# Optimization experiments

Hardware: AMD Instinct MI355X
Metric: run time of the kernel (lower is better)

Reference implementation:

```python
import jax, jax.numpy as jnp
import numpy as np

RATIO = 2
GROUPS = 4


def conv1x1(x, w, b):
    # x: (B,C,H,W), w: (O,C), b: (O,)
    return jnp.einsum('bchw,oc->bohw', x, w) + b[None, :, None, None]


def pixel_unshuffle(x, r):
    # out[b, c*r*r + i*r + j, h, w] = x[b, c, h*r+i, w*r+j]  (torch semantics)
    B, C, H, W = x.shape
    x = x.reshape(B, C, H // r, r, W // r, r)
    x = x.transpose(0, 1, 3, 5, 2, 4)
    return x.reshape(B, C * r * r, H // r, W // r)


def grid_sample_bilinear_border(img, grid):
    # img: (N,C,H,W); grid: (N,Ho,Wo,2), grid[...,0]=x coord, grid[...,1]=y coord in [-1,1]
    # align_corners=False, padding_mode='border' (torch: clip coord to border, then bilinear)
    N, C, H, W = img.shape
    ix = ((grid[..., 0] + 1.0) * W - 1.0) * 0.5
    iy = ((grid[..., 1] + 1.0) * H - 1.0) * 0.5
    ix = jnp.clip(ix, 0.0, W - 1.0)
    iy = jnp.clip(iy, 0.0, H - 1.0)
    x0 = jnp.floor(ix)
    y0 = jnp.floor(iy)
    wx = (ix - x0)[:, None]  # (N,1,Ho,Wo) broadcast over C
    wy = (iy - y0)[:, None]
    x0i = x0.astype(jnp.int32)
    y0i = y0.astype(jnp.int32)
    x1i = jnp.minimum(x0i + 1, W - 1)
    y1i = jnp.minimum(y0i + 1, H - 1)
    gather = jax.vmap(lambda im, yy, xx: im[:, yy, xx])  # (C,Ho,Wo) per batch
    v00 = gather(img, y0i, x0i)
    v01 = gather(img, y0i, x1i)
    v10 = gather(img, y1i, x0i)
    v11 = gather(img, y1i, x1i)
    return (v00 * (1 - wx) * (1 - wy) + v01 * wx * (1 - wy)
            + v10 * (1 - wx) * wy + v11 * wx * wy)


def setup_inputs() -> dict:
    key = jax.random.key(0)
    k1, k2, k3 = jax.random.split(key, 3)
    B, C, H, W = 16, 64, 256, 256
    c_out = 2 * (GROUPS // RATIO ** 2)  # = 2
    x = jax.random.normal(k1, (B, C, H, W), jnp.float32)
    w_off = jax.random.normal(k2, (c_out, C), jnp.float32) * 0.001
    b_off = jnp.zeros((c_out,), jnp.float32)
    w_sc = jax.random.normal(k3, (c_out, C), jnp.float32) * 0.001
    b_sc = jnp.zeros((c_out,), jnp.float32)
    return {"x": x, "w_off": w_off, "b_off": b_off, "w_sc": w_sc, "b_sc": b_sc}


def reference(x, w_off, b_off, w_sc, b_sc):
    B, Cin, H, W = x.shape  # H,W divisible by RATIO -> replicate pad is a no-op
    # forward_lp with dyScope=True
    off = conv1x1(x, w_off, b_off)
    off = jax.nn.sigmoid(conv1x1(x, w_sc, b_sc)) * 0.5 * off
    off = pixel_unshuffle(off, RATIO)            # (B, 2*GROUPS, h, w)
    h, w = off.shape[2], off.shape[3]
    # x: 'b (c grp) h w -> (b grp) c h w'
    cg = Cin // GROUPS
    xg = x.reshape(B, cg, GROUPS, H, W).transpose(0, 2, 1, 3, 4).reshape(B * GROUPS, cg, H, W)
    # offset: 'b (grp two) h w -> (b grp) h w two'
    offg = off.reshape(B, GROUPS, 2, h, w).transpose(0, 1, 3, 4, 2).reshape(B * GROUPS, h, w, 2)
    # pos: stack(meshgrid(h_coord, w_coord)) -> channel 0 = h_coord, channel 1 = w_coord
    hc = jnp.arange(h, dtype=x.dtype) + 0.5
    wc = jnp.arange(w, dtype=x.dtype) + 0.5
    pos = jnp.stack(jnp.meshgrid(hc, wc, indexing='ij'), axis=-1)[None]  # (1,h,w,2)
    norm = jnp.array([w, h], dtype=x.dtype)  # normalizer = [w, h]
    grid = 2.0 * (pos + offg) / norm - 1.0
    out = grid_sample_bilinear_border(xg, grid)  # (B*GROUPS, cg, h, w)
    out = out.reshape(B, GROUPS, cg, h, w).transpose(0, 2, 1, 3, 4).reshape(B, Cin, h, w)
    return out, offg
```

## Files before the change

kernel.cpp:

```cpp
#include <hip/hip_runtime.h>
#include <math.h>

#define BATCH 16
#define CIN   64
#define HIN   256
#define WIN   256
#define HOUT  128
#define WOUT  128
#define NPIX  (HIN * WIN)
#define NPIXO (HOUT * WOUT)
#define OUT0_SIZE ((size_t)BATCH * CIN * HOUT * WOUT)

__global__ __launch_bounds__(256) void k_fused(
    const float* __restrict__ x,
    const float* __restrict__ w_off, const float* __restrict__ b_off,
    const float* __restrict__ w_sc,  const float* __restrict__ b_sc,
    float* __restrict__ out, float* __restrict__ offg)
{
    __shared__ float  sw[256];
    __shared__ float2 soff[4][16][17];
    __shared__ float  sval[4][16][272];

    int t = threadIdx.x;
    sw[t] = (t < 128) ? w_off[t] : w_sc[t - 128];

    int blk  = blockIdx.x;
    int b    = blk >> 6;
    int tile = blk & 63;
    int hh0  = (tile >> 3) * 16;
    int ww0  = (tile & 7) * 16;

    int row = t >> 4, col = t & 15;
    int hh = hh0 + row, ww = ww0 + col;

    const float* xb = x + (size_t)b * CIN * NPIX + (2 * hh) * WIN + 2 * ww;

    float aA0[2][2] = {{0,0},{0,0}}, aA1[2][2] = {{0,0},{0,0}};
    float aS0[2][2] = {{0,0},{0,0}}, aS1[2][2] = {{0,0},{0,0}};

    __syncthreads();

    #pragma unroll 8
    for (int c = 0; c < CIN; ++c) {
        const float* xc = xb + (size_t)c * NPIX;
        float2 r0 = *reinterpret_cast<const float2*>(xc);
        float2 r1 = *reinterpret_cast<const float2*>(xc + WIN);
        float wo0 = sw[c], wo1 = sw[64 + c], ws0 = sw[128 + c], ws1 = sw[192 + c];
        aA0[0][0] += r0.x * wo0;  aA0[0][1] += r0.y * wo0;
        aA0[1][0] += r1.x * wo0;  aA0[1][1] += r1.y * wo0;
        aA1[0][0] += r0.x * wo1;  aA1[0][1] += r0.y * wo1;
        aA1[1][0] += r1.x * wo1;  aA1[1][1] += r1.y * wo1;
        aS0[0][0] += r0.x * ws0;  aS0[0][1] += r0.y * ws0;
        aS0[1][0] += r1.x * ws0;  aS0[1][1] += r1.y * ws0;
        aS1[0][0] += r0.x * ws1;  aS1[0][1] += r0.y * ws1;
        aS1[1][0] += r1.x * ws1;  aS1[1][1] += r1.y * ws1;
    }

    float bo0 = b_off[0], bo1 = b_off[1];
    float bs0 = b_sc[0],  bs1 = b_sc[1];

    float og[4][2];
    #pragma unroll
    for (int i = 0; i < 2; ++i) {
        #pragma unroll
        for (int j = 0; j < 2; ++j) {
            float g0 = 1.0f / (1.0f + __expf(-(aS0[i][j] + bs0)));
            float g1 = 1.0f / (1.0f + __expf(-(aS1[i][j] + bs1)));
            og[i][j]     = g0 * 0.5f * (aA0[i][j] + bo0);
            og[2 + i][j] = g1 * 0.5f * (aA1[i][j] + bo1);
        }
    }

    #pragma unroll
    for (int g = 0; g < 4; ++g) {
        float2 vv = make_float2(og[g][0], og[g][1]);
        soff[g][row][col] = vv;
        size_t oi = ((size_t)((b * 4 + g) * HOUT + hh)) * WOUT + ww;
        *reinterpret_cast<float2*>(offg + 2 * oi) = vv;
    }
    __syncthreads();

    int hl = t & 15, wl = t >> 4;
    int shh = hh0 + hl, sww = ww0 + wl;
    const float* xg = x + (size_t)b * CIN * NPIX;

    #pragma unroll
    for (int g = 0; g < 4; ++g) {
        float2 off = soff[g][hl][wl];
        float ix = 2.0f * ((float)shh + 0.5f + off.x) - 0.5f;
        float iy = 2.0f * ((float)sww + 0.5f + off.y) - 0.5f;
        ix = fminf(fmaxf(ix, 0.0f), (float)(WIN - 1));
        iy = fminf(fmaxf(iy, 0.0f), (float)(HIN - 1));

        float x0f = floorf(ix), y0f = floorf(iy);
        float wx = ix - x0f, wy = iy - y0f;
        int x0 = (int)x0f, y0 = (int)y0f;
        int x1 = min(x0 + 1, WIN - 1);
        int y1 = min(y0 + 1, HIN - 1);

        float w00 = (1.0f - wx) * (1.0f - wy);
        float w01 = wx * (1.0f - wy);
        float w10 = (1.0f - wx) * wy;
        float w11 = wx * wy;

        int i00 = y0 * WIN + x0, i01 = y0 * WIN + x1;
        int i10 = y1 * WIN + x0, i11 = y1 * WIN + x1;

        const float* xgc = xg + (size_t)g * NPIX;
        #pragma unroll 4
        for (int c = 0; c < 16; ++c) {
            const float* xc = xgc + (size_t)c * 4 * NPIX;
            float v = xc[i00] * w00 + xc[i01] * w01
                    + xc[i10] * w10 + xc[i11] * w11;
            sval[g][c][hl * 17 + wl] = v;
        }
    }
    __syncthreads();

    int sh = t >> 4, sc = t & 15;
    float* ob = out + (((size_t)b * CIN) * HOUT + (hh0 + sh)) * WOUT + (ww0 + sc);
    #pragma unroll
    for (int g = 0; g < 4; ++g) {
        #pragma unroll 4
        for (int c = 0; c < 16; ++c)
            ob[(size_t)(c * 4 + g) * NPIXO] = sval[g][c][sh * 17 + sc];
    }
}

extern "C" void kernel_launch(void* const* d_in, const int* in_sizes, int n_in,
                              void* d_out, int out_size, void* d_ws, size_t ws_size,
                              hipStream_t stream) {
    const float* x     = (const float*)d_in[0];
    const float* w_off = (const float*)d_in[1];
    const float* b_off = (const float*)d_in[2];
    const float* w_sc  = (const float*)d_in[3];
    const float* b_sc  = (const float*)d_in[4];

    float* out  = (float*)d_out;
    float* offg = out + OUT0_SIZE;

    k_fused<<<1024, 256, 0, stream>>>(x, w_off, b_off, w_sc, b_sc, out, offg);
}
```

Measured before the change: 102.3 us.

## Stage transposed tile pairs in bf16 LDS and sample from shared memory

Each block now handles a pair of transposed 16x16 input tiles (p,q) and (q,p), because the reference's swapped h/w coordinate convention makes output (h,w) sample near input (2w,2h). Both tiles are staged in LDS as bf16, so the 1x1 convs and the bilinear gathers mostly read shared memory, with a global-memory fallback when a wave's samples fall outside the staged tile. Output is transposed through wave shuffles and written with nontemporal stores. The bf16 rounding of x changes the numerics of both the offsets and the sampled outputs, which risks tolerance failures. Large LDS use and the uneven triangular tile-pair grid also change occupancy and load balance.

```diff
diff --git a/kernel.cpp b/kernel.cpp
--- a/kernel.cpp
+++ b/kernel.cpp
@@ -9,121 +9,157 @@
 #define WOUT  128
 #define NPIX  (HIN * WIN)
 #define NPIXO (HOUT * WOUT)
-#define OUT0_SIZE ((size_t)BATCH * CIN * HOUT * WOUT)
+#define OUT0_SIZE ((size_t)BATCH * CIN * NPIXO)
 
-__global__ __launch_bounds__(256) void k_fused(
+#define NTILE 16
+#define NPAIR 136
+#define SQ_CH 256
+#define SQ_SZ (64 * SQ_CH)
+
+typedef __attribute__((ext_vector_type(4))) float f32x4;
+
+__device__ __forceinline__ unsigned short f2bf(float f) {
+    unsigned u = __float_as_uint(f);
+    return (unsigned short)((u + 0x7FFFu + ((u >> 16) & 1u)) >> 16);
+}
+
+__global__ __launch_bounds__(256, 2) void k_fused(
     const float* __restrict__ x,
     const float* __restrict__ w_off, const float* __restrict__ b_off,
     const float* __restrict__ w_sc,  const float* __restrict__ b_sc,
     float* __restrict__ out, float* __restrict__ offg)
 {
-    __shared__ float  sw[256];
-    __shared__ float2 soff[4][16][17];
-    __shared__ float  sval[4][16][272];
+    __shared__ unsigned short sq[2 * SQ_SZ];
+    __shared__ float soff[2][4][8][8][2];
+    __shared__ float sw[256];
 
-    int t = threadIdx.x;
+    const int t = threadIdx.x;
     sw[t] = (t < 128) ? w_off[t] : w_sc[t - 128];
 
-    int blk  = blockIdx.x;
-    int b    = blk >> 6;
-    int tile = blk & 63;
-    int hh0  = (tile >> 3) * 16;
-    int ww0  = (tile & 7) * 16;
+    int blk = blockIdx.x;
+    int b = blk / NPAIR;
+    int u = blk - b * NPAIR;
+    int p = 0;
+    while (u >= NTILE - p) { u -= NTILE - p; ++p; }
+    const int q = p + u;
+    const bool diag = (p == q);
+    const int nsq = diag ? 1 : 2;
 
-    int row = t >> 4, col = t & 15;
-    int hh = hh0 + row, ww = ww0 + col;
+    const float* xb = x + (size_t)b * CIN * NPIX;
+    const int rb[2] = {16 * p, 16 * q};
+    const int cb[2] = {16 * q, 16 * p};
 
-    const float* xb = x + (size_t)b * CIN * NPIX + (2 * hh) * WIN + 2 * ww;
-
-    float aA0[2][2] = {{0,0},{0,0}}, aA1[2][2] = {{0,0},{0,0}};
-    float aS0[2][2] = {{0,0},{0,0}}, aS1[2][2] = {{0,0},{0,0}};
-
-    __syncthreads();
-
-    #pragma unroll 8
-    for (int c = 0; c < CIN; ++c) {
-        const float* xc = xb + (size_t)c * NPIX;
-        float2 r0 = *reinterpret_cast<const float2*>(xc);
-        float2 r1 = *reinterpret_cast<const float2*>(xc + WIN);
-        float wo0 = sw[c], wo1 = sw[64 + c], ws0 = sw[128 + c], ws1 = sw[192 + c];
-        aA0[0][0] += r0.x * wo0;  aA0[0][1] += r0.y * wo0;
-        aA0[1][0] += r1.x * wo0;  aA0[1][1] += r1.y * wo0;
-        aA1[0][0] += r0.x * wo1;  aA1[0][1] += r0.y * wo1;
-        aA1[1][0] += r1.x * wo1;  aA1[1][1] += r1.y * wo1;
-        aS0[0][0] += r0.x * ws0;  aS0[0][1] += r0.y * ws0;
-        aS0[1][0] += r1.x * ws0;  aS0[1][1] += r1.y * ws0;
-        aS1[0][0] += r0.x * ws1;  aS1[0][1] += r0.y * ws1;
-        aS1[1][0] += r1.x * ws1;  aS1[1][1] += r1.y * ws1;
-    }
-
-    float bo0 = b_off[0], bo1 = b_off[1];
-    float bs0 = b_sc[0],  bs1 = b_sc[1];
-
-    float og[4][2];
-    #pragma unroll
-    for (int i = 0; i < 2; ++i) {
-        #pragma unroll
-        for (int j = 0; j < 2; ++j) {
-            float g0 = 1.0f / (1.0f + __expf(-(aS0[i][j] + bs0)));
-            float g1 = 1.0f / (1.0f + __expf(-(aS1[i][j] + bs1)));
-            og[i][j]     = g0 * 0.5f * (aA0[i][j] + bo0);
-            og[2 + i][j] = g1 * 0.5f * (aA1[i][j] + bo1);
-        }
-    }
-
-    #pragma unroll
-    for (int g = 0; g < 4; ++g) {
-        float2 vv = make_float2(og[g][0], og[g][1]);
-        soff[g][row][col] = vv;
-        size_t oi = ((size_t)((b * 4 + g) * HOUT + hh)) * WOUT + ww;
-        *reinterpret_cast<float2*>(offg + 2 * oi) = vv;
+    for (int it = 0; it < 16 * nsq; ++it) {
+        int idx = it * 256 + t;
+        int s   = idx >> 12;
+        int rem = idx & 4095;
+        int ch  = rem >> 6;
+        int row = (rem >> 2) & 15;
+        int q4  = rem & 3;
+        const float* gp = xb + (size_t)ch * NPIX
+                        + (size_t)(rb[s] + row) * WIN + cb[s] + q4 * 4;
+        f32x4 f = *reinterpret_cast<const f32x4*>(gp);
+        ushort4 h;
+        h.x = f2bf(f[0]); h.y = f2bf(f[1]); h.z = f2bf(f[2]); h.w = f2bf(f[3]);
+        *reinterpret_cast<ushort4*>(
+            &sq[s * SQ_SZ + ch * SQ_CH + row * 16 + q4 * 4]) = h;
     }
     __syncthreads();
 
-    int hl = t & 15, wl = t >> 4;
-    int shh = hh0 + hl, sww = ww0 + wl;
-    const float* xg = x + (size_t)b * CIN * NPIX;
-
-    #pragma unroll
-    for (int g = 0; g < 4; ++g) {
-        float2 off = soff[g][hl][wl];
-        float ix = 2.0f * ((float)shh + 0.5f + off.x) - 0.5f;
-        float iy = 2.0f * ((float)sww + 0.5f + off.y) - 0.5f;
-        ix = fminf(fmaxf(ix, 0.0f), (float)(WIN - 1));
-        iy = fminf(fmaxf(iy, 0.0f), (float)(HIN - 1));
-
-        float x0f = floorf(ix), y0f = floorf(iy);
-        float wx = ix - x0f, wy = iy - y0f;
-        int x0 = (int)x0f, y0 = (int)y0f;
-        int x1 = min(x0 + 1, WIN - 1);
-        int y1 = min(y0 + 1, HIN - 1);
-
-        float w00 = (1.0f - wx) * (1.0f - wy);
-        float w01 = wx * (1.0f - wy);
-        float w10 = (1.0f - wx) * wy;
-        float w11 = wx * wy;
-
-        int i00 = y0 * WIN + x0, i01 = y0 * WIN + x1;
-        int i10 = y1 * WIN + x0, i11 = y1 * WIN + x1;
-
-        const float* xgc = xg + (size_t)g * NPIX;
-        #pragma unroll 4
-        for (int c = 0; c < 16; ++c) {
-            const float* xc = xgc + (size_t)c * 4 * NPIX;
-            float v = xc[i00] * w00 + xc[i01] * w01
-                    + xc[i10] * w10 + xc[i11] * w11;
-            sval[g][c][hl * 17 + wl] = v;
+    const float bo0 = b_off[0], bo1 = b_off[1];
+    const float bs0 = b_sc[0],  bs1 = b_sc[1];
+    for (int s = 0; s < nsq; ++s) {
+        const int r = t >> 4, c = t & 15;
+        const unsigned short* sp = &sq[s * SQ_SZ + r * 16 + c];
+        float a0 = 0, a1 = 0, z0 = 0, z1 = 0;
+        #pragma unroll 16
+        for (int ch = 0; ch < 64; ++ch) {
+            float xv = __uint_as_float((unsigned)sp[ch * SQ_CH] << 16);
+            a0 += xv * sw[ch];       a1 += xv * sw[64 + ch];
+            z0 += xv * sw[128 + ch]; z1 += xv * sw[192 + ch];
         }
+        float o0 = 0.5f * (a0 + bo0) / (1.0f + __expf(-(z0 + bs0)));
+        float o1 = 0.5f * (a1 + bo1) / (1.0f + __expf(-(z1 + bs1)));
+        const int i = r & 1, j = c & 1, hl = r >> 1, wl = c >> 1;
+        soff[s][i][hl][wl][j]     = o0;
+        soff[s][2 + i][hl][wl][j] = o1;
+        const int hh = (s ? 8 * q : 8 * p) + hl;
+        const int ww = (s ? 8 * p : 8 * q) + wl;
+        size_t o0i = (((size_t)(b * 4 + i))     * HOUT + hh) * WOUT + ww;
+        size_t o1i = (((size_t)(b * 4 + 2 + i)) * HOUT + hh) * WOUT + ww;
+        __builtin_nontemporal_store(o0, offg + 2 * o0i + j);
+        __builtin_nontemporal_store(o1, offg + 2 * o1i + j);
     }
     __syncthreads();
 
-    int sh = t >> 4, sc = t & 15;
-    float* ob = out + (((size_t)b * CIN) * HOUT + (hh0 + sh)) * WOUT + (ww0 + sc);
-    #pragma unroll
-    for (int g = 0; g < 4; ++g) {
-        #pragma unroll 4
-        for (int c = 0; c < 16; ++c)
-            ob[(size_t)(c * 4 + g) * NPIXO] = sval[g][c][sh * 17 + sc];
+    const int lane = t & 63;
+    const int half = (t >> 6) & 1;
+    const int tile = t >> 7;
+    if (!(diag && tile == 1)) {
+        const int hl = lane & 7, wl = lane >> 3;
+        const int hb = tile ? 8 * q : 8 * p;
+        const int wb = tile ? 8 * p : 8 * q;
+        const int gs = diag ? 0 : (1 - tile);
+        const int RB = rb[gs], CB = cb[gs];
+        const int hh = hb + hl, ww = wb + wl;
+        const int srcl = ((lane & 7) << 3) | (lane >> 3);
+        const int hh2 = hb + (lane >> 3), ww2 = wb + (lane & 7);
+        float* outp = out + (size_t)b * CIN * NPIXO
+                    + (size_t)hh2 * WOUT + ww2;
+
+        #pragma unroll
+        for (int g = 0; g < 4; ++g) {
+            const float ox = soff[tile][g][hl][wl][0];
+            const float oy = soff[tile][g][hl][wl][1];
+            float ix = 2.0f * (float)hh + 0.5f + 2.0f * ox;
+            float iy = 2.0f * (float)ww + 0.5f + 2.0f * oy;
+            ix = fminf(fmaxf(ix, 0.0f), 255.0f);
+            iy = fminf(fmaxf(iy, 0.0f), 255.0f);
+            float x0f = floorf(ix), y0f = floorf(iy);
+            float wx = ix - x0f, wy = iy - y0f;
+            int x0 = (int)x0f, y0 = (int)y0f;
+            int x1 = min(x0 + 1, WIN - 1);
+            int y1 = min(y0 + 1, HIN - 1);
+            float w00 = (1.0f - wx) * (1.0f - wy);
+            float w01 = wx * (1.0f - wy);
+            float w10 = (1.0f - wx) * wy;
+            float w11 = wx * wy;
+
+            const int xl = x0 - CB, yl = y0 - RB;
+            bool ok = (xl >= 0) & (xl <= 14) & ((xl & 1) == 0)
+                    & (yl >= 0) & (yl <= 14)
+                    & (x1 == x0 + 1) & (y1 == y0 + 1);
+
+            if (__all(ok)) {
+                const unsigned short* spg = &sq[gs * SQ_SZ + yl * 16 + xl];
+                #pragma unroll
+                for (int ci = 0; ci < 8; ++ci) {
+                    const int ch = 4 * (half * 8 + ci) + g;
+                    const unsigned short* cp = spg + ch * SQ_CH;
+                    unsigned v0 = *reinterpret_cast<const unsigned*>(cp);
+                    unsigned v1 = *reinterpret_cast<const unsigned*>(cp + 16);
+                    float f00 = __uint_as_float(v0 << 16);
+                    float f01 = __uint_as_float(v0 & 0xFFFF0000u);
+                    float f10 = __uint_as_float(v1 << 16);
+                    float f11 = __uint_as_float(v1 & 0xFFFF0000u);
+                    float v = f00 * w00 + f01 * w01 + f10 * w10 + f11 * w11;
+                    float vt = __shfl(v, srcl, 64);
+                    __builtin_nontemporal_store(vt, outp + (size_t)ch * NPIXO);
+                }
+            } else {
+                int i00 = y0 * WIN + x0, i01 = y0 * WIN + x1;
+                int i10 = y1 * WIN + x0, i11 = y1 * WIN + x1;
+                #pragma unroll
+                for (int ci = 0; ci < 8; ++ci) {
+                    const int ch = 4 * (half * 8 + ci) + g;
+                    const float* xc = xb + (size_t)ch * NPIX;
+                    float v = xc[i00] * w00 + xc[i01] * w01
+                            + xc[i10] * w10 + xc[i11] * w11;
+                    float vt = __shfl(v, srcl, 64);
+                    __builtin_nontemporal_store(vt, outp + (size_t)ch * NPIXO);
+                }
+            }
+        }
     }
 }
 
@@ -139,5 +175,6 @@
     float* out  = (float*)d_out;
     float* offg = out + OUT0_SIZE;
 
-    k_fused<<<1024, 256, 0, stream>>>(x, w_off, b_off, w_sc, b_sc, out, offg);
+    k_fused<<<BATCH * NPAIR, 256, 0, stream>>>(
+        x, w_off, b_off, w_sc, b_sc, out, offg);
 }
```

Measured after the change: 128.8 us. 1.26x slower.
